# Kernel optimization log

Measured on AMD Instinct MI355X. Metric: run time of the kernel, lower is better.

Reference implementation:

```python
import jax, jax.numpy as jnp
import numpy as np

ALPHA = 2.0
MARGIN = 0.05


def setup_inputs() -> dict:
    key = jax.random.key(0)
    k1, k2, k3, k4 = jax.random.split(key, 4)
    B, n_dim, n_classes = 8192, 2048, 100
    x = jax.random.normal(k1, (B, 1, n_dim), dtype=jnp.float32)
    W = jax.random.normal(k2, (n_dim, n_classes), dtype=jnp.float32) * 0.02
    anchors = jax.random.normal(k3, (n_classes, 1, n_dim), dtype=jnp.float32)
    y = jax.random.randint(k4, (B,), 0, n_classes)
    return {"x": x, "W": W, "anchors": anchors, "y": y}


def reference(x, W, anchors, y):
    # x: (B, 1, n_dim), W: (n_dim, C) linear classifier, anchors: (C, 1, n_dim), y: (B,)
    B = x.shape[0]
    n_classes = W.shape[1]
    xf = x.reshape(B, -1)                               # (B, n_dim)
    px = xf @ W                                         # (B, C) logits
    logp = jax.nn.log_softmax(px, axis=-1)
    ce_x = -jnp.take_along_axis(logp, y[:, None], axis=1)[:, 0]   # (B,)
    onehot = jax.nn.one_hot(y, n_classes, dtype=px.dtype)
    # d(sum ce_x)/dx for a linear classifier: (softmax - onehot) @ W^T (create_graph analogue: differentiable)
    grad_x = (jax.nn.softmax(px, axis=-1) - onehot) @ W.T          # (B, n_dim)

    af = anchors.reshape(n_classes, -1)                 # (C, n_dim)
    pa = af @ W                                         # (C, C), targets = arange(C)
    grad_a = (jax.nn.softmax(pa, axis=-1) - jnp.eye(n_classes, dtype=pa.dtype)) @ W.T  # (C, n_dim)

    # get_anchor_batch: detached gather of grad_a by label
    anchor_batch = jax.lax.stop_gradient(grad_a[y])     # (B, n_dim)
    # get_negative_batch (var='all'): for each i, sum of grad_x[j] over j with y_j != y_i (detached)
    cls_sum = jax.ops.segment_sum(grad_x, y, num_segments=n_classes)   # (C, n_dim)
    negative_batch = jax.lax.stop_gradient(grad_x.sum(axis=0) - cls_sum[y])  # (B, n_dim)

    anchor_positive = jnp.sum(grad_x * anchor_batch, axis=-1)        # (B,)
    anchor_negative = jnp.sum(negative_batch * anchor_batch, axis=-1)  # (B,)
    triplet = anchor_negative - anchor_positive + MARGIN
    loss = ce_x + ALPHA * triplet
    return jnp.mean(loss)
```

## Files before the change

kernel.cpp:

```cpp
#include <hip/hip_runtime.h>
#include <math.h>

#define NB      8192
#define ND      2048
#define NC      100
#define NCP     112
#define ALPHA_  2.0f
#define MARGIN_ 0.05f

typedef short bf16x8 __attribute__((ext_vector_type(8)));
typedef float f32x4 __attribute__((ext_vector_type(4)));

static __device__ __forceinline__ unsigned short f2bf(float f) {
  unsigned u = __float_as_uint(f);
  u += 0x7FFFu + ((u >> 16) & 1u);
  return (unsigned short)(u >> 16);
}

__global__ __launch_bounds__(256) void k_prepW(const float* __restrict__ W,
                                               unsigned short* __restrict__ Wtf) {
  const int f   = blockIdx.x * 256 + threadIdx.x;
  const int ws  = f / 448;
  const int rem = f - ws * 448;
  const int i   = rem >> 6;
  const int l   = rem & 63;
  const int col = i * 16 + (l & 15);
  const int k0  = ws * 32 + (l >> 4) * 8;
  bf16x8 v;
#pragma unroll
  for (int j = 0; j < 8; ++j)
    v[j] = (short)((col < NC) ? f2bf(W[(size_t)(k0 + j) * NC + col]) : 0);
  *(bf16x8*)(Wtf + (size_t)f * 8) = v;
}

__global__ __launch_bounds__(512) void k_prepG(const unsigned short* __restrict__ Wtf,
                                               const float* __restrict__ A,
                                               float* __restrict__ G2,
                                               float* __restrict__ pa2) {
  __shared__ float red[8][8][64];
  const int t    = threadIdx.x;
  const int w    = t >> 6;
  const int lane = t & 63;
  const int ti   = blockIdx.x / 7;
  const int tj   = blockIdx.x % 7;
  const int arow = ti * 16 + (lane & 15);

  f32x4 accG = {0.f, 0.f, 0.f, 0.f};
  f32x4 accP = {0.f, 0.f, 0.f, 0.f};
#pragma unroll
  for (int s = 0; s < 8; ++s) {
    const int ws = w * 8 + s;
    const bf16x8 afr = *(const bf16x8*)(Wtf + (size_t)(ws * 7 + ti) * 512 + lane * 8);
    const bf16x8 bfr = *(const bf16x8*)(Wtf + (size_t)(ws * 7 + tj) * 512 + lane * 8);
    accG = __builtin_amdgcn_mfma_f32_16x16x32_bf16(afr, bfr, accG, 0, 0, 0);
    bf16x8 aa;
    if (arow < NC) {
      const float* __restrict__ ar =
          A + (size_t)arow * ND + ws * 32 + (lane >> 4) * 8;
      const float4 v0 = *(const float4*)(ar);
      const float4 v1 = *(const float4*)(ar + 4);
      aa[0] = (short)f2bf(v0.x); aa[1] = (short)f2bf(v0.y);
      aa[2] = (short)f2bf(v0.z); aa[3] = (short)f2bf(v0.w);
      aa[4] = (short)f2bf(v1.x); aa[5] = (short)f2bf(v1.y);
      aa[6] = (short)f2bf(v1.z); aa[7] = (short)f2bf(v1.w);
    } else {
#pragma unroll
      for (int q = 0; q < 8; ++q) aa[q] = 0;
    }
    accP = __builtin_amdgcn_mfma_f32_16x16x32_bf16(aa, bfr, accP, 0, 0, 0);
  }
#pragma unroll
  for (int rg = 0; rg < 4; ++rg) {
    red[w][rg][lane]     = accG[rg];
    red[w][4 + rg][lane] = accP[rg];
  }
  __syncthreads();
  if (w < 2) {
    const int vb = w * 4;
    float* __restrict__ dst = (w == 0) ? G2 : pa2;
#pragma unroll
    for (int rg = 0; rg < 4; ++rg) {
      float s = 0.f;
#pragma unroll
      for (int w2 = 0; w2 < 8; ++w2) s += red[w2][vb + rg][lane];
      const int row = ti * 16 + (lane >> 4) * 4 + rg;
      dst[row * NCP + tj * 16 + (lane & 15)] = s;
    }
  }
}

__global__ __launch_bounds__(128) void k_prep2(const float* __restrict__ G2,
                                               const float* __restrict__ pa2,
                                               float* __restrict__ Ut,
                                               float* __restrict__ cls_ap) {
  __shared__ float vals[128];
  __shared__ float tl[128];
  const int cp = blockIdx.x;
  const int t  = threadIdx.x;
  if (cp == 0) cls_ap[t] = 0.f;
  const float v = (t < NC) ? pa2[cp * NCP + t] : -INFINITY;
  vals[t] = v;
  __syncthreads();
  float m = -INFINITY;
  for (int c = 0; c < NC; ++c) m = fmaxf(m, vals[c]);
  float se = 0.f;
  for (int c = 0; c < NC; ++c) se += __expf(vals[c] - m);
  tl[t] = (t < NC) ? (__expf(v - m) / se - (t == cp ? 1.f : 0.f)) : 0.f;
  __syncthreads();
  if (t < NC) {
    float u = 0.f;
    for (int c = 0; c < NC; ++c) u = fmaf(G2[c * NCP + t], tl[c], u);
    Ut[cp * NC + t] = u;
  }
}

__global__ __launch_bounds__(512, 4) void k_main(const float* __restrict__ X,
                                                 const unsigned short* __restrict__ Wtf,
                                                 const int* __restrict__ Y,
                                                 const float* __restrict__ Ut,
                                                 float* __restrict__ S_part,
                                                 float* __restrict__ rowce,
                                                 float* __restrict__ rowap) {
  __shared__ __align__(16) char smem[65536];
  const int t    = threadIdx.x;
  const int w    = t >> 6;
  const int lane = t & 63;
  const int row0 = blockIdx.x * 16;
  char* __restrict__ wbase = smem + w * 8192;

  const unsigned short* __restrict__ bp0 =
      Wtf + (size_t)(w * 8 * 7) * 512 + lane * 8;
  bf16x8 cur[7], nxt[7];
#pragma unroll
  for (int i = 0; i < 7; ++i) cur[i] = *(const bf16x8*)(bp0 + i * 512);

  {
    const int srow = lane >> 2;
    const int sc   = lane & 3;
    const float* __restrict__ xr =
        X + (size_t)(row0 + srow) * ND + w * 256 + sc * 8;
    const int wsz = (srow & 7) << 4;
#pragma unroll
    for (int j = 0; j < 8; ++j) {
      const float4 v0 = *(const float4*)(xr + j * 32);
      const float4 v1 = *(const float4*)(xr + j * 32 + 4);
      bf16x8 p;
      p[0] = (short)f2bf(v0.x); p[1] = (short)f2bf(v0.y);
      p[2] = (short)f2bf(v0.z); p[3] = (short)f2bf(v0.w);
      p[4] = (short)f2bf(v1.x); p[5] = (short)f2bf(v1.y);
      p[6] = (short)f2bf(v1.z); p[7] = (short)f2bf(v1.w);
      *(bf16x8*)(wbase + srow * 512 + ((sc * 16 + j * 64) ^ wsz)) = p;
    }
  }

  const int r = lane & 15;
  const int g = lane >> 4;

  f32x4 acc[7];
  const f32x4 z = {0.f, 0.f, 0.f, 0.f};
#pragma unroll
  for (int i = 0; i < 7; ++i) acc[i] = z;

  const char* __restrict__ abase = wbase + r * 512;
  const int asz = (r & 7) << 4;
#pragma unroll
  for (int s = 0; s < 8; ++s) {
    const bf16x8 xf = *(const bf16x8*)(abase + ((s * 64 + g * 16) ^ asz));
    if (s < 7) {
      const unsigned short* __restrict__ bpn = bp0 + (size_t)(s + 1) * 7 * 512;
#pragma unroll
      for (int i = 0; i < 7; ++i) nxt[i] = *(const bf16x8*)(bpn + i * 512);
    }
#pragma unroll
    for (int i = 0; i < 7; ++i)
      acc[i] = __builtin_amdgcn_mfma_f32_16x16x32_bf16(xf, cur[i], acc[i], 0, 0, 0);
#pragma unroll
    for (int i = 0; i < 7; ++i) cur[i] = nxt[i];
  }
  __syncthreads();

  float* __restrict__ redp = (float*)smem;
  float* __restrict__ sp   = (float*)(smem + 57344);
#pragma unroll
  for (int i = 0; i < 7; ++i)
#pragma unroll
    for (int j = 0; j < 4; ++j)
      redp[(w * 7 + i) * 256 + j * 64 + lane] = acc[i][j];
  if (t < NCP) sp[t] = 0.f;
  __syncthreads();

  if (w < 4) {
    const int j = w;
    float v[7];
#pragma unroll
    for (int i = 0; i < 7; ++i) {
      float s = 0.f;
#pragma unroll
      for (int w2 = 0; w2 < 8; ++w2)
        s += redp[(w2 * 7 + i) * 256 + j * 64 + lane];
      v[i] = s;
    }
    const bool v6  = (96 + r) < NC;
    const int  row = row0 + g * 4 + j;
    const int  yr  = Y[row];

    float m = -INFINITY;
#pragma unroll
    for (int i = 0; i < 6; ++i) m = fmaxf(m, v[i]);
    if (v6) m = fmaxf(m, v[6]);
#pragma unroll
    for (int off = 8; off > 0; off >>= 1) m = fmaxf(m, __shfl_xor(m, off));

    float e[7];
    float se = 0.f, py = 0.f;
#pragma unroll
    for (int i = 0; i < 7; ++i) {
      const bool valid = (i < 6) | v6;
      e[i] = valid ? __expf(v[i] - m) : 0.f;
      se += e[i];
      if (i * 16 + r == yr) py = v[i];
    }
#pragma unroll
    for (int off = 8; off > 0; off >>= 1) {
      se += __shfl_xor(se, off);
      py += __shfl_xor(py, off);
    }
    const float ce  = m + __logf(se) - py;
    const float inv = 1.f / se;

    const float* __restrict__ uty = Ut + yr * NC;
    float ap = 0.f;
    float s[7];
#pragma unroll
    for (int i = 0; i < 7; ++i) {
      const int col = i * 16 + r;
      s[i] = e[i] * inv - (col == yr ? 1.f : 0.f);
      const float u = ((i < 6) | v6) ? uty[col] : 0.f;
      ap = fmaf(s[i], u, ap);
    }
#pragma unroll
    for (int off = 8; off > 0; off >>= 1) ap += __shfl_xor(ap, off);

    if (r == 0) {
      rowce[row] = ce;
      rowap[row] = ap;
    }
#pragma unroll
    for (int i = 0; i < 7; ++i) atomicAdd(&sp[i * 16 + r], s[i]);
  }
  __syncthreads();
  if (t < NCP) S_part[(size_t)t * 512 + blockIdx.x] = sp[t];
}

__global__ __launch_bounds__(256) void k_red(const int* __restrict__ Y,
                                             const float* __restrict__ S_part,
                                             const float* __restrict__ rowce,
                                             const float* __restrict__ rowap,
                                             float* __restrict__ stot,
                                             float* __restrict__ sums,
                                             float* __restrict__ cls_ap) {
  __shared__ float red[256];
  const int bid = blockIdx.x;
  const int t   = threadIdx.x;
  if (bid < NCP) {
    float s = S_part[(size_t)bid * 512 + t] + S_part[(size_t)bid * 512 + 256 + t];
    red[t] = s;
    __syncthreads();
    for (int off = 128; off > 0; off >>= 1) {
      if (t < off) red[t] += red[t + off];
      __syncthreads();
    }
    if (t == 0) stot[bid] = red[0];
  } else if (bid < 114) {
    const float* __restrict__ src = (bid == 112) ? rowce : rowap;
    float s = 0.f;
    for (int i = t; i < NB; i += 256) s += src[i];
    red[t] = s;
    __syncthreads();
    for (int off = 128; off > 0; off >>= 1) {
      if (t < off) red[t] += red[t + off];
      __syncthreads();
    }
    if (t == 0) sums[bid - 112] = red[0];
  } else {
    const int base = (bid - 114) * 2048;
#pragma unroll
    for (int q = 0; q < 8; ++q) {
      const int i = base + q * 256 + t;
      atomicAdd(&cls_ap[Y[i]], rowap[i]);
    }
  }
}

__global__ __launch_bounds__(256) void k_final(const int* __restrict__ Y,
                                               const float* __restrict__ Ut,
                                               const float* __restrict__ stot,
                                               const float* __restrict__ sums,
                                               const float* __restrict__ cls_ap,
                                               float* __restrict__ out) {
  __shared__ int   hist[NC];
  __shared__ float st[NC];
  __shared__ float red2[256];
  const int t = threadIdx.x;
  if (t < NC) { hist[t] = 0; st[t] = stot[t]; }
  __syncthreads();
  for (int i = t; i < NB; i += 256) atomicAdd(&hist[Y[i]], 1);
  __syncthreads();
  float part = 0.f;
  if (t < NC) {
    float dot = 0.f;
    for (int r = 0; r < NC; ++r) dot = fmaf(st[r], Ut[t * NC + r], dot);
    part = (float)hist[t] * (dot - cls_ap[t]);
  }
  red2[t] = part;
  __syncthreads();
  for (int off = 128; off > 0; off >>= 1) {
    if (t < off) red2[t] += red2[t + off];
    __syncthreads();
  }
  if (t == 0) {
    out[0] = (sums[0] + ALPHA_ * (red2[0] - sums[1] + (float)NB * MARGIN_)) /
             (float)NB;
  }
}

extern "C" void kernel_launch(void* const* d_in, const int* in_sizes, int n_in,
                              void* d_out, int out_size, void* d_ws,
                              size_t ws_size, hipStream_t stream) {
  const float* X = (const float*)d_in[0];
  const float* W = (const float*)d_in[1];
  const float* A = (const float*)d_in[2];
  const int*   Y = (const int*)d_in[3];
  float* out = (float*)d_out;
  char*  ws  = (char*)d_ws;

  float*          G2     = (float*)(ws + 0);
  float*          pa2    = (float*)(ws + 50176);
  float*          Ut     = (float*)(ws + 100352);
  float*          cls_ap = (float*)(ws + 140800);
  float*          stot   = (float*)(ws + 141312);
  float*          sums   = (float*)(ws + 141824);
  unsigned short* Wtf    = (unsigned short*)(ws + 147456);
  float*          S_part = (float*)(ws + 606208);
  float*          rowce  = (float*)(ws + 835584);
  float*          rowap  = (float*)(ws + 868352);

  k_prepW<<<112, 256, 0, stream>>>(W, Wtf);
  k_prepG<<<49, 512, 0, stream>>>(Wtf, A, G2, pa2);
  k_prep2<<<NC, 128, 0, stream>>>(G2, pa2, Ut, cls_ap);
  k_main<<<NB / 16, 512, 0, stream>>>(X, Wtf, Y, Ut, S_part, rowce, rowap);
  k_red<<<118, 256, 0, stream>>>(Y, S_part, rowce, rowap, stot, sums, cls_ap);
  k_final<<<1, 256, 0, stream>>>(Y, Ut, stot, sums, cls_ap, out);
}
```

Measured before the change: 68.81 us.

## Process 32 rows per block with 16 waves reusing each W fragment twice

The main kernel moves to 1024-thread blocks covering 32 rows, each wave owning a 128-wide K slice. Every W fragment loaded from global memory now feeds two MFMAs, one per 16-row half, so W traffic per row is halved. The explicit double-buffered prefetch of W is dropped, and the cross-wave reduction now runs twice through 128KB of LDS. In exchange there is one block per CU, the reduction sums over 16 waves instead of 8, and more barriers are added, so less latency can be hidden.

```diff
diff --git a/kernel.cpp b/kernel.cpp
--- a/kernel.cpp
+++ b/kernel.cpp
@@ -114,142 +114,151 @@
   }
 }
 
-__global__ __launch_bounds__(512, 4) void k_main(const float* __restrict__ X,
-                                                 const unsigned short* __restrict__ Wtf,
-                                                 const int* __restrict__ Y,
-                                                 const float* __restrict__ Ut,
-                                                 float* __restrict__ S_part,
-                                                 float* __restrict__ rowce,
-                                                 float* __restrict__ rowap) {
-  __shared__ __align__(16) char smem[65536];
+__global__ __launch_bounds__(1024) void k_main(const float* __restrict__ X,
+                                               const unsigned short* __restrict__ Wtf,
+                                               const int* __restrict__ Y,
+                                               const float* __restrict__ Ut,
+                                               float* __restrict__ S_part,
+                                               float* __restrict__ rowce,
+                                               float* __restrict__ rowap) {
+  __shared__ __align__(16) char smem[131072];
   const int t    = threadIdx.x;
   const int w    = t >> 6;
   const int lane = t & 63;
-  const int row0 = blockIdx.x * 16;
+  const int row0 = blockIdx.x * 32;
   char* __restrict__ wbase = smem + w * 8192;
 
-  const unsigned short* __restrict__ bp0 =
-      Wtf + (size_t)(w * 8 * 7) * 512 + lane * 8;
-  bf16x8 cur[7], nxt[7];
-#pragma unroll
-  for (int i = 0; i < 7; ++i) cur[i] = *(const bf16x8*)(bp0 + i * 512);
-
   {
-    const int srow = lane >> 2;
-    const int sc   = lane & 3;
+    const int srow = lane >> 1;
+    const int sc   = lane & 1;
     const float* __restrict__ xr =
-        X + (size_t)(row0 + srow) * ND + w * 256 + sc * 8;
+        X + (size_t)(row0 + srow) * ND + w * 128 + sc * 8;
     const int wsz = (srow & 7) << 4;
-#pragma unroll
-    for (int j = 0; j < 8; ++j) {
-      const float4 v0 = *(const float4*)(xr + j * 32);
-      const float4 v1 = *(const float4*)(xr + j * 32 + 4);
-      bf16x8 p;
-      p[0] = (short)f2bf(v0.x); p[1] = (short)f2bf(v0.y);
-      p[2] = (short)f2bf(v0.z); p[3] = (short)f2bf(v0.w);
-      p[4] = (short)f2bf(v1.x); p[5] = (short)f2bf(v1.y);
-      p[6] = (short)f2bf(v1.z); p[7] = (short)f2bf(v1.w);
-      *(bf16x8*)(wbase + srow * 512 + ((sc * 16 + j * 64) ^ wsz)) = p;
+    float4 va[4];
+#pragma unroll
+    for (int jb = 0; jb < 4; ++jb) {
+      const int j0 = jb * 2, j1 = jb * 2 + 1;
+      va[0] = *(const float4*)(xr + j0 * 16);
+      va[1] = *(const float4*)(xr + j0 * 16 + 4);
+      va[2] = *(const float4*)(xr + j1 * 16);
+      va[3] = *(const float4*)(xr + j1 * 16 + 4);
+      bf16x8 p0, p1;
+      p0[0] = (short)f2bf(va[0].x); p0[1] = (short)f2bf(va[0].y);
+      p0[2] = (short)f2bf(va[0].z); p0[3] = (short)f2bf(va[0].w);
+      p0[4] = (short)f2bf(va[1].x); p0[5] = (short)f2bf(va[1].y);
+      p0[6] = (short)f2bf(va[1].z); p0[7] = (short)f2bf(va[1].w);
+      p1[0] = (short)f2bf(va[2].x); p1[1] = (short)f2bf(va[2].y);
+      p1[2] = (short)f2bf(va[2].z); p1[3] = (short)f2bf(va[2].w);
+      p1[4] = (short)f2bf(va[3].x); p1[5] = (short)f2bf(va[3].y);
+      p1[6] = (short)f2bf(va[3].z); p1[7] = (short)f2bf(va[3].w);
+      *(bf16x8*)(wbase + srow * 256 + ((sc * 16 + j0 * 32) ^ wsz)) = p0;
+      *(bf16x8*)(wbase + srow * 256 + ((sc * 16 + j1 * 32) ^ wsz)) = p1;
     }
   }
 
   const int r = lane & 15;
   const int g = lane >> 4;
 
-  f32x4 acc[7];
+  f32x4 acc[7][2];
   const f32x4 z = {0.f, 0.f, 0.f, 0.f};
 #pragma unroll
-  for (int i = 0; i < 7; ++i) acc[i] = z;
-
-  const char* __restrict__ abase = wbase + r * 512;
+  for (int i = 0; i < 7; ++i) { acc[i][0] = z; acc[i][1] = z; }
+
+  const char* __restrict__ abase = wbase + r * 256;
   const int asz = (r & 7) << 4;
 #pragma unroll
-  for (int s = 0; s < 8; ++s) {
-    const bf16x8 xf = *(const bf16x8*)(abase + ((s * 64 + g * 16) ^ asz));
-    if (s < 7) {
-      const unsigned short* __restrict__ bpn = bp0 + (size_t)(s + 1) * 7 * 512;
-#pragma unroll
-      for (int i = 0; i < 7; ++i) nxt[i] = *(const bf16x8*)(bpn + i * 512);
-    }
+  for (int s = 0; s < 4; ++s) {
+    const int ko = (s * 64 + g * 16) ^ asz;
+    const bf16x8 xf0 = *(const bf16x8*)(abase + ko);
+    const bf16x8 xf1 = *(const bf16x8*)(abase + 4096 + ko);
+    const unsigned short* __restrict__ bp =
+        Wtf + (size_t)((w * 4 + s) * 7) * 512 + lane * 8;
+    bf16x8 bf[7];
+#pragma unroll
+    for (int i = 0; i < 7; ++i) bf[i] = *(const bf16x8*)(bp + i * 512);
+#pragma unroll
+    for (int i = 0; i < 7; ++i) {
+      acc[i][0] = __builtin_amdgcn_mfma_f32_16x16x32_bf16(xf0, bf[i], acc[i][0], 0, 0, 0);
+      acc[i][1] = __builtin_amdgcn_mfma_f32_16x16x32_bf16(xf1, bf[i], acc[i][1], 0, 0, 0);
+    }
+  }
+  __syncthreads();
+
+  float* __restrict__ redp = (float*)smem;
+  float* __restrict__ sp   = (float*)(smem + 114688);
+  if (t < NCP) sp[t] = 0.f;
+
+#pragma unroll
+  for (int h = 0; h < 2; ++h) {
 #pragma unroll
     for (int i = 0; i < 7; ++i)
-      acc[i] = __builtin_amdgcn_mfma_f32_16x16x32_bf16(xf, cur[i], acc[i], 0, 0, 0);
-#pragma unroll
-    for (int i = 0; i < 7; ++i) cur[i] = nxt[i];
-  }
-  __syncthreads();
-
-  float* __restrict__ redp = (float*)smem;
-  float* __restrict__ sp   = (float*)(smem + 57344);
-#pragma unroll
-  for (int i = 0; i < 7; ++i)
-#pragma unroll
-    for (int j = 0; j < 4; ++j)
-      redp[(w * 7 + i) * 256 + j * 64 + lane] = acc[i][j];
-  if (t < NCP) sp[t] = 0.f;
-  __syncthreads();
-
-  if (w < 4) {
-    const int j = w;
-    float v[7];
-#pragma unroll
-    for (int i = 0; i < 7; ++i) {
-      float s = 0.f;
-#pragma unroll
-      for (int w2 = 0; w2 < 8; ++w2)
-        s += redp[(w2 * 7 + i) * 256 + j * 64 + lane];
-      v[i] = s;
-    }
-    const bool v6  = (96 + r) < NC;
-    const int  row = row0 + g * 4 + j;
-    const int  yr  = Y[row];
-
-    float m = -INFINITY;
-#pragma unroll
-    for (int i = 0; i < 6; ++i) m = fmaxf(m, v[i]);
-    if (v6) m = fmaxf(m, v[6]);
-#pragma unroll
-    for (int off = 8; off > 0; off >>= 1) m = fmaxf(m, __shfl_xor(m, off));
-
-    float e[7];
-    float se = 0.f, py = 0.f;
-#pragma unroll
-    for (int i = 0; i < 7; ++i) {
-      const bool valid = (i < 6) | v6;
-      e[i] = valid ? __expf(v[i] - m) : 0.f;
-      se += e[i];
-      if (i * 16 + r == yr) py = v[i];
-    }
-#pragma unroll
-    for (int off = 8; off > 0; off >>= 1) {
-      se += __shfl_xor(se, off);
-      py += __shfl_xor(py, off);
-    }
-    const float ce  = m + __logf(se) - py;
-    const float inv = 1.f / se;
-
-    const float* __restrict__ uty = Ut + yr * NC;
-    float ap = 0.f;
-    float s[7];
-#pragma unroll
-    for (int i = 0; i < 7; ++i) {
-      const int col = i * 16 + r;
-      s[i] = e[i] * inv - (col == yr ? 1.f : 0.f);
-      const float u = ((i < 6) | v6) ? uty[col] : 0.f;
-      ap = fmaf(s[i], u, ap);
-    }
-#pragma unroll
-    for (int off = 8; off > 0; off >>= 1) ap += __shfl_xor(ap, off);
-
-    if (r == 0) {
-      rowce[row] = ce;
-      rowap[row] = ap;
-    }
-#pragma unroll
-    for (int i = 0; i < 7; ++i) atomicAdd(&sp[i * 16 + r], s[i]);
-  }
-  __syncthreads();
-  if (t < NCP) S_part[(size_t)t * 512 + blockIdx.x] = sp[t];
+#pragma unroll
+      for (int j = 0; j < 4; ++j)
+        redp[(w * 7 + i) * 256 + j * 64 + lane] = acc[i][h][j];
+    __syncthreads();
+
+    if (w < 4) {
+      const int j = w;
+      float v[7];
+#pragma unroll
+      for (int i = 0; i < 7; ++i) {
+        float s = 0.f;
+#pragma unroll
+        for (int w2 = 0; w2 < 16; ++w2)
+          s += redp[(w2 * 7 + i) * 256 + j * 64 + lane];
+        v[i] = s;
+      }
+      const bool v6  = (96 + r) < NC;
+      const int  row = row0 + h * 16 + g * 4 + j;
+      const int  yr  = Y[row];
+
+      float m = -INFINITY;
+#pragma unroll
+      for (int i = 0; i < 6; ++i) m = fmaxf(m, v[i]);
+      if (v6) m = fmaxf(m, v[6]);
+#pragma unroll
+      for (int off = 8; off > 0; off >>= 1) m = fmaxf(m, __shfl_xor(m, off));
+
+      float e[7];
+      float se = 0.f, py = 0.f;
+#pragma unroll
+      for (int i = 0; i < 7; ++i) {
+        const bool valid = (i < 6) | v6;
+        e[i] = valid ? __expf(v[i] - m) : 0.f;
+        se += e[i];
+        if (i * 16 + r == yr) py = v[i];
+      }
+#pragma unroll
+      for (int off = 8; off > 0; off >>= 1) {
+        se += __shfl_xor(se, off);
+        py += __shfl_xor(py, off);
+      }
+      const float ce  = m + __logf(se) - py;
+      const float inv = 1.f / se;
+
+      const float* __restrict__ uty = Ut + yr * NC;
+      float ap = 0.f;
+      float s[7];
+#pragma unroll
+      for (int i = 0; i < 7; ++i) {
+        const int col = i * 16 + r;
+        s[i] = e[i] * inv - (col == yr ? 1.f : 0.f);
+        const float u = ((i < 6) | v6) ? uty[col] : 0.f;
+        ap = fmaf(s[i], u, ap);
+      }
+#pragma unroll
+      for (int off = 8; off > 0; off >>= 1) ap += __shfl_xor(ap, off);
+
+      if (r == 0) {
+        rowce[row] = ce;
+        rowap[row] = ap;
+      }
+#pragma unroll
+      for (int i = 0; i < 7; ++i) atomicAdd(&sp[i * 16 + r], s[i]);
+    }
+    __syncthreads();
+  }
+  if (t < NCP) S_part[(size_t)t * 256 + blockIdx.x] = sp[t];
 }
 
 __global__ __launch_bounds__(256) void k_red(const int* __restrict__ Y,
@@ -263,8 +272,7 @@
   const int bid = blockIdx.x;
   const int t   = threadIdx.x;
   if (bid < NCP) {
-    float s = S_part[(size_t)bid * 512 + t] + S_part[(size_t)bid * 512 + 256 + t];
-    red[t] = s;
+    red[t] = S_part[(size_t)bid * 256 + t];
     __syncthreads();
     for (int off = 128; off > 0; off >>= 1) {
       if (t < off) red[t] += red[t + off];
@@ -342,13 +350,13 @@
   float*          sums   = (float*)(ws + 141824);
   unsigned short* Wtf    = (unsigned short*)(ws + 147456);
   float*          S_part = (float*)(ws + 606208);
-  float*          rowce  = (float*)(ws + 835584);
-  float*          rowap  = (float*)(ws + 868352);
+  float*          rowce  = (float*)(ws + 720896);
+  float*          rowap  = (float*)(ws + 753664);
 
   k_prepW<<<112, 256, 0, stream>>>(W, Wtf);
   k_prepG<<<49, 512, 0, stream>>>(Wtf, A, G2, pa2);
   k_prep2<<<NC, 128, 0, stream>>>(G2, pa2, Ut, cls_ap);
-  k_main<<<NB / 16, 512, 0, stream>>>(X, Wtf, Y, Ut, S_part, rowce, rowap);
+  k_main<<<NB / 32, 1024, 0, stream>>>(X, Wtf, Y, Ut, S_part, rowce, rowap);
   k_red<<<118, 256, 0, stream>>>(Y, S_part, rowce, rowap, stot, sums, cls_ap);
   k_final<<<1, 256, 0, stream>>>(Y, Ut, stot, sums, cls_ap, out);
 }
```

Measured after the change: 76.42 us. 1.11x slower.

## Fuse reduction and final kernels into main kernel via last-block completion counter

Applied to the files above, without the earlier changes.

Removes the separate k_red and k_final launches. k_main now accumulates ce, ap and per-class ap with atomics, and the last block to finish (found through an atomic done counter) reduces S_part and computes the final loss. The label histogram moves into k_prep2 and the accumulator zeroing into k_prepW. This saves two kernel launches and their dependency gaps, at the cost of global atomics and a serialized tail executed by a single block.

```diff
diff --git a/kernel.cpp b/kernel.cpp
--- a/kernel.cpp
+++ b/kernel.cpp
@@ -17,9 +17,13 @@
   return (unsigned short)(u >> 16);
 }
 
+
 __global__ __launch_bounds__(256) void k_prepW(const float* __restrict__ W,
-                                               unsigned short* __restrict__ Wtf) {
-  const int f   = blockIdx.x * 256 + threadIdx.x;
+                                               unsigned short* __restrict__ Wtf,
+                                               float* __restrict__ ACC) {
+  const int t = threadIdx.x;
+  if (blockIdx.x == 0) ACC[t] = 0.f;
+  const int f   = blockIdx.x * 256 + t;
   const int ws  = f / 448;
   const int rem = f - ws * 448;
   const int i   = rem >> 6;
@@ -91,13 +95,17 @@
 
 __global__ __launch_bounds__(128) void k_prep2(const float* __restrict__ G2,
                                                const float* __restrict__ pa2,
+                                               const int* __restrict__ Y,
                                                float* __restrict__ Ut,
-                                               float* __restrict__ cls_ap) {
+                                               int* __restrict__ hist) {
   __shared__ float vals[128];
   __shared__ float tl[128];
   const int cp = blockIdx.x;
   const int t  = threadIdx.x;
-  if (cp == 0) cls_ap[t] = 0.f;
+  {
+    const int i = cp * 82 + t;
+    if (t < 82 && i < NB) atomicAdd(&hist[Y[i]], 1);
+  }
   const float v = (t < NC) ? pa2[cp * NCP + t] : -INFINITY;
   vals[t] = v;
   __syncthreads();
@@ -119,9 +127,15 @@
                                                  const int* __restrict__ Y,
                                                  const float* __restrict__ Ut,
                                                  float* __restrict__ S_part,
-                                                 float* __restrict__ rowce,
-                                                 float* __restrict__ rowap) {
+                                                 float* __restrict__ ACC,
+                                                 float* __restrict__ out) {
   __shared__ __align__(16) char smem[65536];
+  __shared__ bool lastFlag;
+  float* __restrict__ cls_ap = ACC;
+  float* __restrict__ sums   = ACC + 112;
+  const int* __restrict__ hist = (const int*)ACC + 128;
+  int* __restrict__ done       = (int*)ACC + 240;
+
   const int t    = threadIdx.x;
   const int w    = t >> 6;
   const int lane = t & 63;
@@ -186,7 +200,7 @@
 #pragma unroll
     for (int j = 0; j < 4; ++j)
       redp[(w * 7 + i) * 256 + j * 64 + lane] = acc[i][j];
-  if (t < NCP) sp[t] = 0.f;
+  if (t < NCP + 2) sp[t] = 0.f;
   __syncthreads();
 
   if (w < 4) {
@@ -242,79 +256,45 @@
     for (int off = 8; off > 0; off >>= 1) ap += __shfl_xor(ap, off);
 
     if (r == 0) {
-      rowce[row] = ce;
-      rowap[row] = ap;
+      atomicAdd(&sp[NCP], ce);
+      atomicAdd(&sp[NCP + 1], ap);
+      atomicAdd(&cls_ap[yr], ap);
     }
 #pragma unroll
     for (int i = 0; i < 7; ++i) atomicAdd(&sp[i * 16 + r], s[i]);
   }
   __syncthreads();
   if (t < NCP) S_part[(size_t)t * 512 + blockIdx.x] = sp[t];
-}
-
-__global__ __launch_bounds__(256) void k_red(const int* __restrict__ Y,
-                                             const float* __restrict__ S_part,
-                                             const float* __restrict__ rowce,
-                                             const float* __restrict__ rowap,
-                                             float* __restrict__ stot,
-                                             float* __restrict__ sums,
-                                             float* __restrict__ cls_ap) {
-  __shared__ float red[256];
-  const int bid = blockIdx.x;
-  const int t   = threadIdx.x;
-  if (bid < NCP) {
-    float s = S_part[(size_t)bid * 512 + t] + S_part[(size_t)bid * 512 + 256 + t];
-    red[t] = s;
-    __syncthreads();
-    for (int off = 128; off > 0; off >>= 1) {
-      if (t < off) red[t] += red[t + off];
-      __syncthreads();
-    }
-    if (t == 0) stot[bid] = red[0];
-  } else if (bid < 114) {
-    const float* __restrict__ src = (bid == 112) ? rowce : rowap;
+  if (t == NCP) atomicAdd(&sums[0], sp[NCP]);
+  if (t == NCP + 1) atomicAdd(&sums[1], sp[NCP + 1]);
+
+  __threadfence();
+  __syncthreads();
+  if (t == 0) lastFlag = (atomicAdd(done, 1) == 511);
+  __syncthreads();
+  if (!lastFlag) return;
+  __threadfence();
+
+  float* __restrict__ stot = (float*)smem;
+  float* __restrict__ red2 = (float*)(smem + 2048);
+  for (int c = w; c < NCP; c += 8) {
     float s = 0.f;
-    for (int i = t; i < NB; i += 256) s += src[i];
-    red[t] = s;
-    __syncthreads();
-    for (int off = 128; off > 0; off >>= 1) {
-      if (t < off) red[t] += red[t + off];
-      __syncthreads();
-    }
-    if (t == 0) sums[bid - 112] = red[0];
-  } else {
-    const int base = (bid - 114) * 2048;
-#pragma unroll
-    for (int q = 0; q < 8; ++q) {
-      const int i = base + q * 256 + t;
-      atomicAdd(&cls_ap[Y[i]], rowap[i]);
-    }
-  }
-}
-
-__global__ __launch_bounds__(256) void k_final(const int* __restrict__ Y,
-                                               const float* __restrict__ Ut,
-                                               const float* __restrict__ stot,
-                                               const float* __restrict__ sums,
-                                               const float* __restrict__ cls_ap,
-                                               float* __restrict__ out) {
-  __shared__ int   hist[NC];
-  __shared__ float st[NC];
-  __shared__ float red2[256];
-  const int t = threadIdx.x;
-  if (t < NC) { hist[t] = 0; st[t] = stot[t]; }
-  __syncthreads();
-  for (int i = t; i < NB; i += 256) atomicAdd(&hist[Y[i]], 1);
+#pragma unroll
+    for (int q = 0; q < 8; ++q) s += S_part[(size_t)c * 512 + q * 64 + lane];
+#pragma unroll
+    for (int off = 32; off > 0; off >>= 1) s += __shfl_xor(s, off);
+    if (lane == 0) stot[c] = s;
+  }
   __syncthreads();
   float part = 0.f;
   if (t < NC) {
     float dot = 0.f;
-    for (int r = 0; r < NC; ++r) dot = fmaf(st[r], Ut[t * NC + r], dot);
+    for (int c = 0; c < NC; ++c) dot = fmaf(stot[c], Ut[t * NC + c], dot);
     part = (float)hist[t] * (dot - cls_ap[t]);
   }
   red2[t] = part;
   __syncthreads();
-  for (int off = 128; off > 0; off >>= 1) {
+  for (int off = 256; off > 0; off >>= 1) {
     if (t < off) red2[t] += red2[t + off];
     __syncthreads();
   }
@@ -337,18 +317,12 @@
   float*          G2     = (float*)(ws + 0);
   float*          pa2    = (float*)(ws + 50176);
   float*          Ut     = (float*)(ws + 100352);
-  float*          cls_ap = (float*)(ws + 140800);
-  float*          stot   = (float*)(ws + 141312);
-  float*          sums   = (float*)(ws + 141824);
+  float*          ACC    = (float*)(ws + 140800);
   unsigned short* Wtf    = (unsigned short*)(ws + 147456);
   float*          S_part = (float*)(ws + 606208);
-  float*          rowce  = (float*)(ws + 835584);
-  float*          rowap  = (float*)(ws + 868352);
-
-  k_prepW<<<112, 256, 0, stream>>>(W, Wtf);
+
+  k_prepW<<<112, 256, 0, stream>>>(W, Wtf, ACC);
   k_prepG<<<49, 512, 0, stream>>>(Wtf, A, G2, pa2);
-  k_prep2<<<NC, 128, 0, stream>>>(G2, pa2, Ut, cls_ap);
-  k_main<<<NB / 16, 512, 0, stream>>>(X, Wtf, Y, Ut, S_part, rowce, rowap);
-  k_red<<<118, 256, 0, stream>>>(Y, S_part, rowce, rowap, stot, sums, cls_ap);
-  k_final<<<1, 256, 0, stream>>>(Y, Ut, stot, sums, cls_ap, out);
-}
+  k_prep2<<<NC, 128, 0, stream>>>(G2, pa2, Y, Ut, (int*)ACC + 128);
+  k_main<<<NB / 16, 512, 0, stream>>>(X, Wtf, Y, Ut, S_part, ACC, out);
+}
```

Result: slower. 145.8 us (+112.0%).

## Merge W prep and Gram/anchor-logit kernels into one FP32 split-K launch

Applied to the files above, without the earlier changes.

Fuses the W bf16 repacking and the W^T W / anchor-logit computation into a single launch. The Gram and anchor logits are now computed in FP32 with an 8-way split-K across 800 blocks, and the partial sums are reduced inside k_prep2. The label histogram moves from the single-block final kernel into k_prep2 using global atomics, and cls_ap plus hist are zeroed by an extra block of the fused kernel. This removes one launch and the serial histogram loop in k_final, at the cost of more partial-buffer traffic and strided scalar W reads.

```diff
diff --git a/kernel.cpp b/kernel.cpp
--- a/kernel.cpp
+++ b/kernel.cpp
@@ -17,88 +17,74 @@
   return (unsigned short)(u >> 16);
 }
 
-__global__ __launch_bounds__(256) void k_prepW(const float* __restrict__ W,
-                                               unsigned short* __restrict__ Wtf) {
-  const int f   = blockIdx.x * 256 + threadIdx.x;
-  const int ws  = f / 448;
-  const int rem = f - ws * 448;
-  const int i   = rem >> 6;
-  const int l   = rem & 63;
-  const int col = i * 16 + (l & 15);
-  const int k0  = ws * 32 + (l >> 4) * 8;
-  bf16x8 v;
-#pragma unroll
-  for (int j = 0; j < 8; ++j)
-    v[j] = (short)((col < NC) ? f2bf(W[(size_t)(k0 + j) * NC + col]) : 0);
-  *(bf16x8*)(Wtf + (size_t)f * 8) = v;
-}
-
-__global__ __launch_bounds__(512) void k_prepG(const unsigned short* __restrict__ Wtf,
+__global__ __launch_bounds__(256) void k_prepA(const float* __restrict__ W,
                                                const float* __restrict__ A,
-                                               float* __restrict__ G2,
-                                               float* __restrict__ pa2) {
-  __shared__ float red[8][8][64];
-  const int t    = threadIdx.x;
-  const int w    = t >> 6;
-  const int lane = t & 63;
-  const int ti   = blockIdx.x / 7;
-  const int tj   = blockIdx.x % 7;
-  const int arow = ti * 16 + (lane & 15);
-
-  f32x4 accG = {0.f, 0.f, 0.f, 0.f};
-  f32x4 accP = {0.f, 0.f, 0.f, 0.f};
-#pragma unroll
-  for (int s = 0; s < 8; ++s) {
-    const int ws = w * 8 + s;
-    const bf16x8 afr = *(const bf16x8*)(Wtf + (size_t)(ws * 7 + ti) * 512 + lane * 8);
-    const bf16x8 bfr = *(const bf16x8*)(Wtf + (size_t)(ws * 7 + tj) * 512 + lane * 8);
-    accG = __builtin_amdgcn_mfma_f32_16x16x32_bf16(afr, bfr, accG, 0, 0, 0);
-    bf16x8 aa;
-    if (arow < NC) {
-      const float* __restrict__ ar =
-          A + (size_t)arow * ND + ws * 32 + (lane >> 4) * 8;
-      const float4 v0 = *(const float4*)(ar);
-      const float4 v1 = *(const float4*)(ar + 4);
-      aa[0] = (short)f2bf(v0.x); aa[1] = (short)f2bf(v0.y);
-      aa[2] = (short)f2bf(v0.z); aa[3] = (short)f2bf(v0.w);
-      aa[4] = (short)f2bf(v1.x); aa[5] = (short)f2bf(v1.y);
-      aa[6] = (short)f2bf(v1.z); aa[7] = (short)f2bf(v1.w);
-    } else {
-#pragma unroll
-      for (int q = 0; q < 8; ++q) aa[q] = 0;
-    }
-    accP = __builtin_amdgcn_mfma_f32_16x16x32_bf16(aa, bfr, accP, 0, 0, 0);
-  }
-#pragma unroll
-  for (int rg = 0; rg < 4; ++rg) {
-    red[w][rg][lane]     = accG[rg];
-    red[w][4 + rg][lane] = accP[rg];
-  }
-  __syncthreads();
-  if (w < 2) {
-    const int vb = w * 4;
-    float* __restrict__ dst = (w == 0) ? G2 : pa2;
-#pragma unroll
-    for (int rg = 0; rg < 4; ++rg) {
-      float s = 0.f;
-#pragma unroll
-      for (int w2 = 0; w2 < 8; ++w2) s += red[w2][vb + rg][lane];
-      const int row = ti * 16 + (lane >> 4) * 4 + rg;
-      dst[row * NCP + tj * 16 + (lane & 15)] = s;
-    }
-  }
-}
-
-__global__ __launch_bounds__(128) void k_prep2(const float* __restrict__ G2,
-                                               const float* __restrict__ pa2,
+                                               unsigned short* __restrict__ Wtf,
+                                               float* __restrict__ Gp,
+                                               float* __restrict__ pap,
+                                               float* __restrict__ zstrip) {
+  __shared__ float wcol[256];
+  __shared__ float arow[256];
+  const int bid = blockIdx.x;
+  const int t   = threadIdx.x;
+  if (bid < 112) {
+    const int f   = bid * 256 + t;
+    const int ws  = f / 448;
+    const int rem = f - ws * 448;
+    const int i   = rem >> 6;
+    const int l   = rem & 63;
+    const int col = i * 16 + (l & 15);
+    const int k0  = ws * 32 + (l >> 4) * 8;
+    bf16x8 v;
+#pragma unroll
+    for (int j = 0; j < 8; ++j)
+      v[j] = (short)((col < NC) ? f2bf(W[(size_t)(k0 + j) * NC + col]) : 0);
+    *(bf16x8*)(Wtf + (size_t)f * 8) = v;
+  } else if (bid < 912) {
+    const int idx = bid - 112;
+    const int r   = idx >> 3;
+    const int ks  = idx & 7;
+    const int k0  = ks * 256;
+    wcol[t] = W[(size_t)(k0 + t) * NC + r];
+    arow[t] = A[(size_t)r * ND + k0 + t];
+    __syncthreads();
+    if (t < NC) {
+      float g = 0.f, p = 0.f;
+#pragma unroll 8
+      for (int kk = 0; kk < 256; ++kk) {
+        const float w = W[(size_t)(k0 + kk) * NC + t];
+        g = fmaf(wcol[kk], w, g);
+        p = fmaf(arow[kk], w, p);
+      }
+      Gp[(size_t)(ks * NC + r) * NCP + t]  = g;
+      pap[(size_t)(ks * NC + r) * NCP + t] = p;
+    }
+  } else {
+    for (int i = t; i < 384; i += 256) zstrip[i] = 0.f;
+  }
+}
+
+__global__ __launch_bounds__(128) void k_prep2(const float* __restrict__ Gp,
+                                               const float* __restrict__ pap,
+                                               const int* __restrict__ Y,
                                                float* __restrict__ Ut,
-                                               float* __restrict__ cls_ap) {
+                                               int* __restrict__ hist) {
   __shared__ float vals[128];
   __shared__ float tl[128];
   const int cp = blockIdx.x;
   const int t  = threadIdx.x;
-  if (cp == 0) cls_ap[t] = 0.f;
-  const float v = (t < NC) ? pa2[cp * NCP + t] : -INFINITY;
+  {
+    const int i = cp * 82 + t;
+    if (t < 82 && i < NB) atomicAdd(&hist[Y[i]], 1);
+  }
+  float v = -INFINITY;
+  if (t < NC) {
+    float s = 0.f;
+#pragma unroll
+    for (int ks = 0; ks < 8; ++ks)
+      s += pap[(size_t)(ks * NC + cp) * NCP + t];
+    v = s;
+  }
   vals[t] = v;
   __syncthreads();
   float m = -INFINITY;
@@ -109,7 +95,12 @@
   __syncthreads();
   if (t < NC) {
     float u = 0.f;
-    for (int c = 0; c < NC; ++c) u = fmaf(G2[c * NCP + t], tl[c], u);
+#pragma unroll
+    for (int ks = 0; ks < 8; ++ks) {
+      const float* __restrict__ gp = Gp + (size_t)ks * NC * NCP;
+#pragma unroll 4
+      for (int c = 0; c < NC; ++c) u = fmaf(gp[c * NCP + t], tl[c], u);
+    }
     Ut[cp * NC + t] = u;
   }
 }
@@ -292,24 +283,21 @@
   }
 }
 
-__global__ __launch_bounds__(256) void k_final(const int* __restrict__ Y,
+__global__ __launch_bounds__(256) void k_final(const int* __restrict__ hist,
                                                const float* __restrict__ Ut,
                                                const float* __restrict__ stot,
                                                const float* __restrict__ sums,
                                                const float* __restrict__ cls_ap,
                                                float* __restrict__ out) {
-  __shared__ int   hist[NC];
   __shared__ float st[NC];
   __shared__ float red2[256];
   const int t = threadIdx.x;
-  if (t < NC) { hist[t] = 0; st[t] = stot[t]; }
-  __syncthreads();
-  for (int i = t; i < NB; i += 256) atomicAdd(&hist[Y[i]], 1);
+  if (t < NC) st[t] = stot[t];
   __syncthreads();
   float part = 0.f;
   if (t < NC) {
     float dot = 0.f;
-    for (int r = 0; r < NC; ++r) dot = fmaf(st[r], Ut[t * NC + r], dot);
+    for (int c = 0; c < NC; ++c) dot = fmaf(st[c], Ut[t * NC + c], dot);
     part = (float)hist[t] * (dot - cls_ap[t]);
   }
   red2[t] = part;
@@ -334,21 +322,21 @@
   float* out = (float*)d_out;
   char*  ws  = (char*)d_ws;
 
-  float*          G2     = (float*)(ws + 0);
-  float*          pa2    = (float*)(ws + 50176);
-  float*          Ut     = (float*)(ws + 100352);
-  float*          cls_ap = (float*)(ws + 140800);
-  float*          stot   = (float*)(ws + 141312);
-  float*          sums   = (float*)(ws + 141824);
-  unsigned short* Wtf    = (unsigned short*)(ws + 147456);
-  float*          S_part = (float*)(ws + 606208);
-  float*          rowce  = (float*)(ws + 835584);
-  float*          rowap  = (float*)(ws + 868352);
-
-  k_prepW<<<112, 256, 0, stream>>>(W, Wtf);
-  k_prepG<<<49, 512, 0, stream>>>(Wtf, A, G2, pa2);
-  k_prep2<<<NC, 128, 0, stream>>>(G2, pa2, Ut, cls_ap);
+  float*          Gp     = (float*)(ws + 0);
+  float*          pap    = (float*)(ws + 358400);
+  float*          Ut     = (float*)(ws + 716800);
+  float*          cls_ap = (float*)(ws + 756800);
+  int*            hist   = (int*)(ws + 757312);
+  float*          sums   = (float*)(ws + 757824);
+  float*          stot   = (float*)(ws + 758336);
+  unsigned short* Wtf    = (unsigned short*)(ws + 760832);
+  float*          S_part = (float*)(ws + 1219584);
+  float*          rowce  = (float*)(ws + 1448960);
+  float*          rowap  = (float*)(ws + 1481728);
+
+  k_prepA<<<913, 256, 0, stream>>>(W, A, Wtf, Gp, pap, cls_ap);
+  k_prep2<<<NC, 128, 0, stream>>>(Gp, pap, Y, Ut, hist);
   k_main<<<NB / 16, 512, 0, stream>>>(X, Wtf, Y, Ut, S_part, rowce, rowap);
   k_red<<<118, 256, 0, stream>>>(Y, S_part, rowce, rowap, stot, sums, cls_ap);
-  k_final<<<1, 256, 0, stream>>>(Y, Ut, stot, sums, cls_ap, out);
-}
+  k_final<<<1, 256, 0, stream>>>(hist, Ut, stot, sums, cls_ap, out);
+}
```

Result: slower. 112.7 us (+63.8%).
